# Performance work log

Hardware: AMD Instinct MI355X
Metric: run time of the kernel (lower is better)

The kernel has to match this reference:

```python
import jax, jax.numpy as jnp
import numpy as np

N, E, B = 16384, 131072, 256
F_IN, HID, HEADS, F_CELL, N_OUT = 78, 128, 10, 954, 2
NEG_SLOPE = 0.2  # PyG GATConv default


def setup_inputs() -> dict:
    key = jax.random.key(0)
    ks = jax.random.split(key, 24)
    rn = lambda k, shape, s=0.05: (jax.random.normal(k, shape, jnp.float32) * s)
    inp = {
        "x": rn(ks[0], (N, F_IN), 1.0),
        "edge_index": jax.random.randint(ks[1], (2, E), 0, N, dtype=jnp.int32),
        "batch": (jnp.arange(N, dtype=jnp.int32) // (N // B)),  # 64 nodes per graph, sorted
        "cell": rn(ks[2], (B, F_CELL), 1.0),
        "W1": rn(ks[3], (F_IN, HEADS * HID)),
        "a_src1": rn(ks[4], (HEADS, HID)),
        "a_dst1": rn(ks[5], (HEADS, HID)),
        "b1": jnp.zeros((HEADS * HID,), jnp.float32),
        # GATConv layer 2: 1280 -> 128, 1 head
        "W2": rn(ks[6], (HEADS * HID, HID)),
        "a_src2": rn(ks[7], (1, HID)),
        "a_dst2": rn(ks[8], (1, HID)),
        "b2": jnp.zeros((HID,), jnp.float32),
        # drug1_fc_g1: 128 -> 128
        "Wg": rn(ks[9], (HID, HID)), "bg": jnp.zeros((HID,), jnp.float32),
        # fc head applied to normalized cell (source applies fc1 to cell: 954 -> 2048)
        "Wf1": rn(ks[10], (F_CELL, 2048)), "bf1": jnp.zeros((2048,), jnp.float32),
        "Wf2": rn(ks[11], (2048, 512)), "bf2": jnp.zeros((512,), jnp.float32),
        "Wf3": rn(ks[12], (512, 128)), "bf3": jnp.zeros((128,), jnp.float32),
        "Wo": rn(ks[13], (128, N_OUT)), "bo": jnp.zeros((N_OUT,), jnp.float32),
    }
    return inp


def _gat_layer(xin, src, dst, W, a_s, a_d, b, heads, ch):
    """PyG GATConv: linear -> per-edge leaky_relu(a_src.h_j + a_dst.h_i) ->
    segment softmax over incoming edges of dst -> scatter-add of alpha * h_src."""
    n = xin.shape[0]
    h = (xin @ W).reshape(n, heads, ch)                       # [N,H,C]
    es = jnp.einsum('nhc,hc->nh', h, a_s)                     # alpha_src per node
    ed = jnp.einsum('nhc,hc->nh', h, a_d)                     # alpha_dst per node
    e = jax.nn.leaky_relu(es[src] + ed[dst], NEG_SLOPE)       # [Etot,H]
    m = jax.ops.segment_max(e, dst, num_segments=n)           # stable softmax max
    w = jnp.exp(e - m[dst])                                   # unnormalized alpha
    denom = jax.ops.segment_sum(w, dst, num_segments=n)       # [N,H]
    num = jax.ops.segment_sum(w[:, :, None] * h[src], dst, num_segments=n)  # [N,H,C]
    out = num / denom[:, :, None]
    return out.reshape(n, heads * ch) + b


def reference(x, edge_index, batch, cell, W1, a_src1, a_dst1, b1,
              W2, a_src2, a_dst2, b2, Wg, bg, Wf1, bf1, Wf2, bf2,
              Wf3, bf3, Wo, bo):
    n = x.shape[0]
    # add self-loops (PyG GATConv default)
    loop = jnp.arange(n, dtype=edge_index.dtype)
    src = jnp.concatenate([edge_index[0], loop])
    dst = jnp.concatenate([edge_index[1], loop])

    x1 = jax.nn.elu(_gat_layer(x, src, dst, W1, a_src1, a_dst1, b1, HEADS, HID))
    x1 = jax.nn.elu(_gat_layer(x1, src, dst, W2, a_src2, a_dst2, b2, 1, HID))
    # global max pool over graphs (batch is sorted, all B segments non-empty)
    x1 = jax.ops.segment_max(x1, batch, num_segments=B)       # [B,128]
    x1 = jax.nn.relu(x1 @ Wg + bg)

    # cell branch: L2 normalize rows, then dense head (dropout = identity in eval)
    celln = cell / jnp.maximum(jnp.linalg.norm(cell, axis=1, keepdims=True), 1e-12)
    xc = jax.nn.relu(celln @ Wf1 + bf1)
    xc = jax.nn.relu(xc @ Wf2 + bf2)
    xc = jax.nn.relu(xc @ Wf3 + bf3)
    out = xc @ Wo + bo                                        # [B,2]
    # source returns only `out`; we also expose the (otherwise-dead) GAT branch
    return jnp.concatenate([x1, out], axis=1)                 # [B,130]
```

## Files before the change

kernel.cpp:

```cpp
#include <hip/hip_runtime.h>
#include <hip/hip_bf16.h>
#include <math.h>

#define N_NODES 16384
#define E_EDGES 131072
#define ETOT (E_EDGES + N_NODES)
#define BGRAPH 256
#define F_INPUT 78
#define KPAD1 96
#define HID 128
#define HEADS 10
#define F1 (HEADS * HID)
#define F_CELL 954
#define KPADC 960
#define NEG_SLOPE 0.2f

typedef __attribute__((ext_vector_type(8))) short frag_t;
typedef __attribute__((ext_vector_type(4))) float f4_t;

static __device__ __forceinline__ unsigned fkey(float f) {
    unsigned b = __float_as_uint(f);
    return (b & 0x80000000u) ? ~b : (b | 0x80000000u);
}
static __device__ __forceinline__ float funkey(unsigned k) {
    unsigned b = (k & 0x80000000u) ? (k ^ 0x80000000u) : ~k;
    return __uint_as_float(b);
}
static __device__ __forceinline__ unsigned short f2bf(float f) {
    __hip_bfloat16 h = __float2bfloat16(f);
    return *(unsigned short*)&h;
}
static __device__ __forceinline__ float bf2f(unsigned short u) {
    return __uint_as_float(((unsigned)u) << 16);
}

template<int WM16, int WN16, int OUT_MODE, int ACT, int HAS_BIAS>
__global__ __launch_bounds__(256) void mfma_gemm(
    const unsigned short* __restrict__ A, const unsigned short* __restrict__ BT,
    const float* __restrict__ bias, void* __restrict__ C,
    float* __restrict__ esp, float* __restrict__ edp,
    int M, int N, int Kpad, int lda, int ldc,
    int za, int zb, int zc, int zbias)
{
    constexpr int BM = 32 * WM16, BN = 32 * WN16;
    __shared__ __align__(16) unsigned short Als[BM * 32];
    __shared__ __align__(16) unsigned short Bls[BN * 32];
    const int z = blockIdx.z;
    A  += (size_t)z * za;
    BT += (size_t)z * zb;
    const int t = threadIdx.x;
    const int wave = t >> 6, lane = t & 63;
    const int wr = (wave >> 1) * (16 * WM16);
    const int wc = (wave & 1) * (16 * WN16);
    const int row0 = blockIdx.y * BM;
    const int col0 = blockIdx.x * BN;

    f4_t acc[WM16][WN16];
#pragma unroll
    for (int m = 0; m < WM16; m++)
#pragma unroll
        for (int n = 0; n < WN16; n++) { acc[m][n] = (f4_t){0.f, 0.f, 0.f, 0.f}; }

    const int lrow = lane & 15, kg = lane >> 4;
    for (int kk = 0; kk < Kpad; kk += 32) {
        for (int i = t; i < BM * 4; i += 256) {
            int r = i >> 2, slot = i & 3;
            uint4 v = *(const uint4*)&A[(size_t)(row0 + r) * lda + kk + slot * 8];
            *(uint4*)&Als[r * 32 + ((slot ^ (r & 3) ^ ((r >> 2) & 3)) * 8)] = v;
        }
        for (int i = t; i < BN * 4; i += 256) {
            int r = i >> 2, slot = i & 3;
            uint4 v = *(const uint4*)&BT[(size_t)(col0 + r) * Kpad + kk + slot * 8];
            *(uint4*)&Bls[r * 32 + ((slot ^ (r & 3) ^ ((r >> 2) & 3)) * 8)] = v;
        }
        __syncthreads();
        frag_t af[WM16], bfr[WN16];
#pragma unroll
        for (int m = 0; m < WM16; m++) {
            int r = wr + m * 16 + lrow;
            af[m] = *(frag_t*)&Als[r * 32 + ((kg ^ (r & 3) ^ ((r >> 2) & 3)) * 8)];
        }
#pragma unroll
        for (int n = 0; n < WN16; n++) {
            int r = wc + n * 16 + lrow;
            bfr[n] = *(frag_t*)&Bls[r * 32 + ((kg ^ (r & 3) ^ ((r >> 2) & 3)) * 8)];
        }
#pragma unroll
        for (int m = 0; m < WM16; m++)
#pragma unroll
            for (int n = 0; n < WN16; n++)
                acc[m][n] = __builtin_amdgcn_mfma_f32_16x16x32_bf16(af[m], bfr[n], acc[m][n], 0, 0, 0);
        __syncthreads();
    }

#pragma unroll
    for (int m = 0; m < WM16; m++) {
#pragma unroll
        for (int n = 0; n < WN16; n++) {
            int col = col0 + wc + n * 16 + lrow;
            float bv = HAS_BIAS ? bias[z * zbias + col] : 0.f;
#pragma unroll
            for (int r = 0; r < 4; r++) {
                int row = row0 + wr + m * 16 + kg * 4 + r;
                float v = acc[m][n][r] + bv;
                if (ACT == 1) v = fmaxf(v, 0.f);
                if (ACT == 2) v = (v > 0.f) ? v : expm1f(v);
                size_t ci = (size_t)row * ldc + (size_t)z * zc + col;
                if (OUT_MODE == 0)      ((float*)C)[ci] = v;
                else if (OUT_MODE == 1) ((unsigned short*)C)[ci] = f2bf(v);
                else {
                    if (col < 10)                  esp[row * 10 + col] = v;
                    else if (col >= 16 && col < 26) edp[row * 10 + (col - 16)] = v;
                }
            }
        }
    }
}

#define S0 1572864
#define S1 122880
#define S2 163840
#define S3 1966080
#define S4 1048576
#define S5 65536
#define S6 16384
#define PREP_TOTAL (S0+S1+S2+S3+S4+S5+S6)

__global__ void prep_weights(const float* __restrict__ x,  const float* __restrict__ W1,
                             const float* __restrict__ W2, const float* __restrict__ Wf1,
                             const float* __restrict__ Wf2, const float* __restrict__ Wf3,
                             const float* __restrict__ Wg,
                             unsigned short* __restrict__ xb,  unsigned short* __restrict__ W1T,
                             unsigned short* __restrict__ W2T, unsigned short* __restrict__ Wf1T,
                             unsigned short* __restrict__ Wf2T, unsigned short* __restrict__ Wf3T,
                             unsigned short* __restrict__ WgT)
{
    int i = blockIdx.x * 256 + threadIdx.x;
    if (i < S0) { int r = i / 96, k = i % 96;
        xb[i] = (k < F_INPUT) ? f2bf(x[r * F_INPUT + k]) : 0; return; }
    i -= S0;
    if (i < S1) { int n = i / 96, k = i % 96;
        W1T[i] = (k < F_INPUT) ? f2bf(W1[(size_t)k * F1 + n]) : 0; return; }
    i -= S1;
    if (i < S2) { int n = i / 1280, k = i % 1280;
        W2T[i] = f2bf(W2[(size_t)k * HID + n]); return; }
    i -= S2;
    if (i < S3) { int n = i / 960, k = i % 960;
        Wf1T[i] = (k < F_CELL) ? f2bf(Wf1[(size_t)k * 2048 + n]) : 0; return; }
    i -= S3;
    if (i < S4) { int n = i / 2048, k = i % 2048;
        Wf2T[i] = f2bf(Wf2[(size_t)k * 512 + n]); return; }
    i -= S4;
    if (i < S5) { int n = i / 512, k = i % 512;
        Wf3T[i] = f2bf(Wf3[(size_t)k * HID + n]); return; }
    i -= S5;
    { int n = i / 128, k = i % 128;
        WgT[i] = f2bf(Wg[(size_t)k * HID + n]); }
}

__global__ void fold1_w(const float* __restrict__ W1, const float* __restrict__ as_,
                        const float* __restrict__ ad_, unsigned short* __restrict__ F1T)
{
    int idx = blockIdx.x * 4 + (threadIdx.x >> 6);
    int l = threadIdx.x & 63;
    int r = idx / 96, k = idx % 96;
    int sd = r >> 4, h = r & 15;
    float p = 0.f;
    if (h < HEADS && k < F_INPUT) {
        const float* a = (sd ? ad_ : as_) + h * HID;
        float2 wv = *(const float2*)&W1[(size_t)k * F1 + h * HID + 2 * l];
        float2 av = *(const float2*)&a[2 * l];
        p = wv.x * av.x + wv.y * av.y;
#pragma unroll
        for (int o = 32; o > 0; o >>= 1) p += __shfl_xor(p, o);
    }
    if (l == 0) F1T[(size_t)r * 96 + k] = f2bf(p);
}

__global__ void hist_dst(const int* __restrict__ ei, int* __restrict__ counts)
{
    int e = blockIdx.x * blockDim.x + threadIdx.x;
    if (e >= ETOT) return;
    int dst = (e < E_EDGES) ? ei[E_EDGES + e] : (e - E_EDGES);
    atomicAdd(&counts[dst], 1);
}

__global__ void scan_counts(const int* __restrict__ counts,
                            int* __restrict__ row_start, int* __restrict__ cursor)
{
    __shared__ int part[256];
    int t = threadIdx.x;
    int base = t * 64;
    int sum = 0;
    for (int i = 0; i < 64; i++) sum += counts[base + i];
    part[t] = sum;
    __syncthreads();
    for (int o = 1; o < 256; o <<= 1) {
        int v = 0;
        if (t >= o) v = part[t - o];
        __syncthreads();
        part[t] += v;
        __syncthreads();
    }
    int run = (t == 0) ? 0 : part[t - 1];
    for (int i = 0; i < 64; i++) {
        row_start[base + i] = run;
        cursor[base + i] = run;
        run += counts[base + i];
    }
    if (t == 255) row_start[N_NODES] = run;
}

__global__ void scatter_csr(const int* __restrict__ ei, int* __restrict__ cursor,
                            int* __restrict__ csr_src)
{
    int e = blockIdx.x * blockDim.x + threadIdx.x;
    if (e >= ETOT) return;
    int src, dst;
    if (e < E_EDGES) { src = ei[e]; dst = ei[E_EDGES + e]; } else { src = dst = e - E_EDGES; }
    int pos = atomicAdd(&cursor[dst], 1);
    csr_src[pos] = src;
}

__global__ void attn_coef2(const unsigned short* __restrict__ H2,
                           const float* __restrict__ as_, const float* __restrict__ ad_,
                           float* __restrict__ es, float* __restrict__ ed)
{
    int n = blockIdx.x * 4 + (threadIdx.x >> 6);
    int l = threadIdx.x & 63;
    unsigned p = *(const unsigned*)&H2[(size_t)n * HID + 2 * l];
    float h0 = bf2f((unsigned short)(p & 0xffffu));
    float h1 = bf2f((unsigned short)(p >> 16));
    float2 av = *(const float2*)&as_[2 * l];
    float2 dv = *(const float2*)&ad_[2 * l];
    float vs = h0 * av.x + h1 * av.y;
    float vd = h0 * dv.x + h1 * dv.y;
#pragma unroll
    for (int o = 32; o > 0; o >>= 1) { vs += __shfl_xor(vs, o); vd += __shfl_xor(vd, o); }
    if (l == 0) { es[n] = vs; ed[n] = vd; }
}

__global__ __launch_bounds__(256) void gat1_agg(
    const int* __restrict__ row_start, const int* __restrict__ csr_src,
    const unsigned* __restrict__ xb32,
    const float* __restrict__ es, const float* __restrict__ ed,
    unsigned* __restrict__ aggb)
{
    const int w = threadIdx.x >> 6, l = threadIdx.x & 63;
    const int n = blockIdx.x * 4 + w;
    const int rs = row_start[n];
    const int deg = row_start[n + 1] - rs;

    __shared__ __align__(16) float w_lds[4][64][12];
    __shared__ int src_lds[4][64];

    float edv[HEADS];
    const float* edp = ed + n * HEADS;
#pragma unroll
    for (int h = 0; h < HEADS; h++) edv[h] = edp[h];

    float acc0[HEADS], acc1[HEADS], den[HEADS];
#pragma unroll
    for (int h = 0; h < HEADS; h++) { acc0[h] = 0.f; acc1[h] = 0.f; den[h] = 0.f; }

    for (int base = 0; base < deg; base += 64) {
        int e = base + l;
        int cnt = min(64, deg - base);
        float wv[HEADS];
        if (e < deg) {
            int s = csr_src[rs + e];
            src_lds[w][l] = s;
            const float* ep = es + s * HEADS;
#pragma unroll
            for (int h = 0; h < HEADS; h++) {
                float v = ep[h] + edv[h];
                v = (v >= 0.f) ? v : NEG_SLOPE * v;
                wv[h] = __expf(v);
            }
        } else {
#pragma unroll
            for (int h = 0; h < HEADS; h++) wv[h] = 0.f;
        }
#pragma unroll
        for (int h = 0; h < HEADS; h++) {
            den[h] += wv[h];
            w_lds[w][l][h] = wv[h];
        }
        asm volatile("" ::: "memory");

        for (int j = 0; j < cnt; j++) {
            int sj = src_lds[w][j];
            unsigned xv = 0;
            if (l < 48) xv = xb32[(size_t)sj * 48 + l];
            float x0 = bf2f((unsigned short)(xv & 0xffffu));
            float x1v = bf2f((unsigned short)(xv >> 16));
            float4 wa = *(const float4*)&w_lds[w][j][0];
            float4 wb = *(const float4*)&w_lds[w][j][4];
            float2 wcv = *(const float2*)&w_lds[w][j][8];
            float ww[HEADS] = {wa.x, wa.y, wa.z, wa.w, wb.x, wb.y, wb.z, wb.w, wcv.x, wcv.y};
#pragma unroll
            for (int h = 0; h < HEADS; h++) {
                acc0[h] = fmaf(ww[h], x0, acc0[h]);
                acc1[h] = fmaf(ww[h], x1v, acc1[h]);
            }
        }
        asm volatile("" ::: "memory");
    }

#pragma unroll
    for (int h = 0; h < HEADS; h++)
#pragma unroll
        for (int o = 32; o > 0; o >>= 1) den[h] += __shfl_xor(den[h], o);

    if (l < 48) {
        unsigned* orow = aggb + (size_t)n * 480;
#pragma unroll
        for (int h = 0; h < HEADS; h++) {
            float inv = 1.f / den[h];
            unsigned lo = f2bf(acc0[h] * inv);
            unsigned hi = f2bf(acc1[h] * inv);
            orow[h * 48 + l] = lo | (hi << 16);
        }
    }
}

__global__ __launch_bounds__(256) void gat2_agg(
    const int* __restrict__ row_start, const int* __restrict__ csr_src,
    const unsigned short* __restrict__ H2,
    const float* __restrict__ es, const float* __restrict__ ed,
    const float* __restrict__ b, float* __restrict__ xout)
{
    const int w = threadIdx.x >> 6, l = threadIdx.x & 63;
    const int n = blockIdx.x * 4 + w;
    const int rs = row_start[n];
    const int deg = row_start[n + 1] - rs;
    const float edv = ed[n];

    float2 acc = {0.f, 0.f};
    float den = 0.f;
    for (int base = 0; base < deg; base += 64) {
        int e = base + l;
        int cnt = min(64, deg - base);
        int s = 0;
        float wv = 0.f;
        if (e < deg) {
            s = csr_src[rs + e];
            float v = es[s] + edv;
            v = (v >= 0.f) ? v : NEG_SLOPE * v;
            wv = __expf(v);
        }
        den += wv;
        for (int j = 0; j < cnt; j++) {
            float wj = __shfl(wv, j);
            int   sj = __shfl(s, j);
            unsigned hp = *(const unsigned*)&H2[(size_t)sj * HID + 2 * l];
            acc.x = fmaf(wj, bf2f((unsigned short)(hp & 0xffffu)), acc.x);
            acc.y = fmaf(wj, bf2f((unsigned short)(hp >> 16)), acc.y);
        }
    }
#pragma unroll
    for (int o = 32; o > 0; o >>= 1) den += __shfl_xor(den, o);

    float inv = 1.f / den;
    float2 bv = *(const float2*)&b[2 * l];
    float v0 = acc.x * inv + bv.x;
    float v1 = acc.y * inv + bv.y;
    float2 ov;
    ov.x = (v0 > 0.f) ? v0 : expm1f(v0);
    ov.y = (v1 > 0.f) ? v1 : expm1f(v1);
    *(float2*)(xout + (size_t)n * HID + 2 * l) = ov;
}

__global__ void pool_max(const float* __restrict__ x2, const int* __restrict__ batch,
                         unsigned* __restrict__ pk)
{
    int idx = blockIdx.x * blockDim.x + threadIdx.x;
    if (idx >= N_NODES * HID) return;
    int n = idx >> 7, c = idx & 127;
    atomicMax(&pk[batch[n] * HID + c], fkey(x2[idx]));
}

__global__ void decode_keys_bf16(const unsigned* __restrict__ pk,
                                 unsigned short* __restrict__ outb, int count)
{
    int i = blockIdx.x * blockDim.x + threadIdx.x;
    if (i < count) outb[i] = f2bf(funkey(pk[i]));
}

__global__ void cell_norm(const float* __restrict__ cell, unsigned short* __restrict__ celln)
{
    int b = blockIdx.x;
    int t = threadIdx.x;
    __shared__ float red[256];
    float s = 0.f;
    for (int c = t; c < F_CELL; c += 256) { float v = cell[(size_t)b * F_CELL + c]; s += v * v; }
    red[t] = s; __syncthreads();
    for (int o = 128; o > 0; o >>= 1) { if (t < o) red[t] += red[t + o]; __syncthreads(); }
    float inv = 1.f / fmaxf(sqrtf(red[0]), 1e-12f);
    for (int c = t; c < KPADC; c += 256) {
        float v = (c < F_CELL) ? cell[(size_t)b * F_CELL + c] * inv : 0.f;
        celln[(size_t)b * KPADC + c] = f2bf(v);
    }
}

__global__ void final_out(const float* __restrict__ xg, const float* __restrict__ xc3,
                          const float* __restrict__ Wo, const float* __restrict__ bo,
                          float* __restrict__ out)
{
    int b = blockIdx.x, t = threadIdx.x;
    float v = xc3[b * HID + t];
    float p0 = v * Wo[t * 2], p1 = v * Wo[t * 2 + 1];
    __shared__ float s[4];
#pragma unroll
    for (int o = 32; o > 0; o >>= 1) { p0 += __shfl_down(p0, o); p1 += __shfl_down(p1, o); }
    if ((t & 63) == 0) { s[(t >> 6) * 2] = p0; s[(t >> 6) * 2 + 1] = p1; }
    __syncthreads();
    out[b * 130 + t] = xg[b * HID + t];
    if (t == 0) {
        out[b * 130 + 128] = s[0] + s[2] + bo[0];
        out[b * 130 + 129] = s[1] + s[3] + bo[1];
    }
}

extern "C" void kernel_launch(void* const* d_in, const int* in_sizes, int n_in,
                              void* d_out, int out_size, void* d_ws, size_t ws_size,
                              hipStream_t stream)
{
    const float* x    = (const float*)d_in[0];
    const int*   ei   = (const int*)d_in[1];
    const int*   batch= (const int*)d_in[2];
    const float* cell = (const float*)d_in[3];
    const float* W1   = (const float*)d_in[4];
    const float* as1  = (const float*)d_in[5];
    const float* ad1  = (const float*)d_in[6];
    const float* b1   = (const float*)d_in[7];
    const float* W2   = (const float*)d_in[8];
    const float* as2  = (const float*)d_in[9];
    const float* ad2  = (const float*)d_in[10];
    const float* b2   = (const float*)d_in[11];
    const float* Wg   = (const float*)d_in[12];
    const float* bg   = (const float*)d_in[13];
    const float* Wf1  = (const float*)d_in[14];
    const float* bf1  = (const float*)d_in[15];
    const float* Wf2  = (const float*)d_in[16];
    const float* bf2  = (const float*)d_in[17];
    const float* Wf3  = (const float*)d_in[18];
    const float* bf3  = (const float*)d_in[19];
    const float* Wo   = (const float*)d_in[20];
    const float* bo   = (const float*)d_in[21];
    float* out = (float*)d_out;

    char* w = (char*)d_ws;
    auto alloc = [&](size_t bytes) { char* p = w; w += (bytes + 255) & ~(size_t)255; return p; };
    unsigned short* xb   = (unsigned short*)alloc((size_t)N_NODES * KPAD1 * 2);
    unsigned short* W1T  = (unsigned short*)alloc((size_t)F1 * KPAD1 * 2);
    unsigned short* F1T  = (unsigned short*)alloc((size_t)32 * KPAD1 * 2);
    unsigned*       aggb = (unsigned*)alloc((size_t)N_NODES * 480 * 4);
    unsigned short* x1   = (unsigned short*)alloc((size_t)N_NODES * F1 * 2);
    unsigned short* W2T  = (unsigned short*)alloc((size_t)HID * F1 * 2);
    unsigned short* H2   = (unsigned short*)alloc((size_t)N_NODES * HID * 2);
    float*    es1  = (float*)alloc((size_t)N_NODES * HEADS * 4);
    float*    ed1  = (float*)alloc((size_t)N_NODES * HEADS * 4);
    float*    es2  = (float*)alloc((size_t)N_NODES * 4);
    float*    ed2  = (float*)alloc((size_t)N_NODES * 4);
    float*    x2   = (float*)alloc((size_t)N_NODES * HID * 4);
    int*      counts    = (int*)alloc((size_t)N_NODES * 4);
    int*      row_start = (int*)alloc((size_t)(N_NODES + 1) * 4);
    int*      cursor    = (int*)alloc((size_t)N_NODES * 4);
    int*      csr_src   = (int*)alloc((size_t)ETOT * 4);
    unsigned* pk   = (unsigned*)alloc((size_t)BGRAPH * HID * 4);
    unsigned short* pooledb = (unsigned short*)alloc((size_t)BGRAPH * HID * 2);
    unsigned short* WgT  = (unsigned short*)alloc((size_t)HID * HID * 2);
    float*    xg   = (float*)alloc((size_t)BGRAPH * HID * 4);
    unsigned short* celln = (unsigned short*)alloc((size_t)BGRAPH * KPADC * 2);
    unsigned short* Wf1T = (unsigned short*)alloc((size_t)2048 * KPADC * 2);
    unsigned short* Wf2T = (unsigned short*)alloc((size_t)512 * 2048 * 2);
    unsigned short* Wf3T = (unsigned short*)alloc((size_t)HID * 512 * 2);
    unsigned short* xc1b = (unsigned short*)alloc((size_t)BGRAPH * 2048 * 2);
    unsigned short* xc2b = (unsigned short*)alloc((size_t)BGRAPH * 512 * 2);
    float*    xc3  = (float*)alloc((size_t)BGRAPH * HID * 4);

    hipMemsetAsync(counts, 0, (size_t)N_NODES * 4, stream);
    hipMemsetAsync(pk,     0, (size_t)BGRAPH * HID * 4, stream);

    dim3 b256(256);
    const int egrid = (ETOT + 255) / 256;

    prep_weights<<<PREP_TOTAL / 256, b256, 0, stream>>>(x, W1, W2, Wf1, Wf2, Wf3, Wg,
                                                        xb, W1T, W2T, Wf1T, Wf2T, Wf3T, WgT);
    fold1_w<<<32 * 96 / 4, b256, 0, stream>>>(W1, as1, ad1, F1T);

    hist_dst<<<egrid, b256, 0, stream>>>(ei, counts);
    scan_counts<<<1, b256, 0, stream>>>(counts, row_start, cursor);
    scatter_csr<<<egrid, b256, 0, stream>>>(ei, cursor, csr_src);

    mfma_gemm<4, 1, 2, 0, 0><<<dim3(1, N_NODES / 128), b256, 0, stream>>>(
        xb, F1T, nullptr, nullptr, es1, ed1, N_NODES, 32, KPAD1, KPAD1, 32, 0, 0, 0, 0);
    gat1_agg<<<N_NODES / 4, b256, 0, stream>>>(row_start, csr_src, (const unsigned*)xb,
                                               es1, ed1, aggb);
    mfma_gemm<4, 4, 1, 2, 1><<<dim3(1, N_NODES / 128, HEADS), b256, 0, stream>>>(
        (const unsigned short*)aggb, W1T, b1, x1, nullptr, nullptr,
        N_NODES, HID, KPAD1, 960, F1, KPAD1, HID * KPAD1, HID, HID);

    mfma_gemm<1, 4, 1, 0, 0><<<dim3(1, N_NODES / 32), b256, 0, stream>>>(
        x1, W2T, nullptr, H2, nullptr, nullptr, N_NODES, HID, F1, F1, HID, 0, 0, 0, 0);
    attn_coef2<<<N_NODES / 4, b256, 0, stream>>>(H2, as2, ad2, es2, ed2);
    gat2_agg<<<N_NODES / 4, b256, 0, stream>>>(row_start, csr_src, H2, es2, ed2, b2, x2);

    pool_max<<<(N_NODES * HID + 255) / 256, b256, 0, stream>>>(x2, batch, pk);
    decode_keys_bf16<<<(BGRAPH * HID + 255) / 256, b256, 0, stream>>>(pk, pooledb, BGRAPH * HID);
    mfma_gemm<2, 2, 0, 1, 1><<<dim3(HID / 64, BGRAPH / 64), b256, 0, stream>>>(
        pooledb, WgT, bg, xg, nullptr, nullptr, BGRAPH, HID, HID, HID, HID, 0, 0, 0, 0);

    cell_norm<<<BGRAPH, b256, 0, stream>>>(cell, celln);
    mfma_gemm<2, 2, 1, 1, 1><<<dim3(2048 / 64, BGRAPH / 64), b256, 0, stream>>>(
        celln, Wf1T, bf1, xc1b, nullptr, nullptr, BGRAPH, 2048, KPADC, KPADC, 2048, 0, 0, 0, 0);
    mfma_gemm<1, 2, 1, 1, 1><<<dim3(512 / 64, BGRAPH / 32), b256, 0, stream>>>(
        xc1b, Wf2T, bf2, xc2b, nullptr, nullptr, BGRAPH, 512, 2048, 2048, 512, 0, 0, 0, 0);
    mfma_gemm<2, 2, 0, 1, 1><<<dim3(HID / 64, BGRAPH / 64), b256, 0, stream>>>(
        xc2b, Wf3T, bf3, xc3, nullptr, nullptr, BGRAPH, HID, 512, 512, HID, 0, 0, 0, 0);

    final_out<<<BGRAPH, 128, 0, stream>>>(xg, xc3, Wo, bo, out);
}
```

Before: 250.7 us.

## Fuse epilogues and small kernels to cut launches and intermediate buffers

Merges weight prep, attention-weight folding and buffer zeroing into one launch, which replaces the two memsets. The layer-2 attention coefficients are computed in the W2 GEMM epilogue, and max-pooling moves into the gat2 aggregation through atomicMax. Cell normalization and key decoding share one kernel, and the final 128->2 projection is folded into the Wf3 GEMM epilogue, which writes straight into the output. This removes about six launches and the full x2 round trip through memory, at the cost of shared-memory atomics in the epilogues and more global atomic contention in the pooling.

```diff
diff --git a/kernel.cpp b/kernel.cpp
--- a/kernel.cpp
+++ b/kernel.cpp
@@ -39,6 +39,7 @@
     const unsigned short* __restrict__ A, const unsigned short* __restrict__ BT,
     const float* __restrict__ bias, void* __restrict__ C,
     float* __restrict__ esp, float* __restrict__ edp,
+    const float* __restrict__ ca, const float* __restrict__ cd,
     int M, int N, int Kpad, int lda, int ldc,
     int za, int zb, int zc, int zbias)
 {
@@ -93,26 +94,76 @@
         __syncthreads();
     }
 
-#pragma unroll
-    for (int m = 0; m < WM16; m++) {
-#pragma unroll
-        for (int n = 0; n < WN16; n++) {
-            int col = col0 + wc + n * 16 + lrow;
-            float bv = HAS_BIAS ? bias[z * zbias + col] : 0.f;
-#pragma unroll
-            for (int r = 0; r < 4; r++) {
-                int row = row0 + wr + m * 16 + kg * 4 + r;
-                float v = acc[m][n][r] + bv;
-                if (ACT == 1) v = fmaxf(v, 0.f);
-                if (ACT == 2) v = (v > 0.f) ? v : expm1f(v);
-                size_t ci = (size_t)row * ldc + (size_t)z * zc + col;
-                if (OUT_MODE == 0)      ((float*)C)[ci] = v;
-                else if (OUT_MODE == 1) ((unsigned short*)C)[ci] = f2bf(v);
-                else {
-                    if (col < 10)                  esp[row * 10 + col] = v;
-                    else if (col >= 16 && col < 26) edp[row * 10 + (col - 16)] = v;
+    if constexpr (OUT_MODE <= 2) {
+#pragma unroll
+        for (int m = 0; m < WM16; m++) {
+#pragma unroll
+            for (int n = 0; n < WN16; n++) {
+                int col = col0 + wc + n * 16 + lrow;
+                float bv = HAS_BIAS ? bias[z * zbias + col] : 0.f;
+#pragma unroll
+                for (int r = 0; r < 4; r++) {
+                    int row = row0 + wr + m * 16 + kg * 4 + r;
+                    float v = acc[m][n][r] + bv;
+                    if (ACT == 1) v = fmaxf(v, 0.f);
+                    if (ACT == 2) v = (v > 0.f) ? v : expm1f(v);
+                    size_t ci = (size_t)row * ldc + (size_t)z * zc + col;
+                    if (OUT_MODE == 0)      ((float*)C)[ci] = v;
+                    else if (OUT_MODE == 1) ((unsigned short*)C)[ci] = f2bf(v);
+                    else {
+                        if (col < 10)                  esp[row * 10 + col] = v;
+                        else if (col >= 16 && col < 26) edp[row * 10 + (col - 16)] = v;
+                    }
                 }
             }
+        }
+    } else if constexpr (OUT_MODE == 3) {
+        __shared__ float esl[BM], edl[BM];
+        if (t < BM) { esl[t] = 0.f; edl[t] = 0.f; }
+        __syncthreads();
+#pragma unroll
+        for (int r = 0; r < 4; r++) {
+            int lr = wr + kg * 4 + r;
+            float pes = 0.f, ped = 0.f;
+#pragma unroll
+            for (int n = 0; n < WN16; n++) {
+                int col = col0 + wc + n * 16 + lrow;
+                float v = acc[0][n][r];
+                ((unsigned short*)C)[(size_t)(row0 + lr) * ldc + col] = f2bf(v);
+                pes = fmaf(v, ca[col], pes);
+                ped = fmaf(v, cd[col], ped);
+            }
+            atomicAdd(&esl[lr], pes);
+            atomicAdd(&edl[lr], ped);
+        }
+        __syncthreads();
+        if (t < BM) { esp[row0 + t] = esl[t]; edp[row0 + t] = edl[t]; }
+    } else {
+        __shared__ float o2l[BM][2];
+        if (t < BM) { o2l[t][0] = 0.f; o2l[t][1] = 0.f; }
+        __syncthreads();
+#pragma unroll
+        for (int m = 0; m < WM16; m++) {
+#pragma unroll
+            for (int r = 0; r < 4; r++) {
+                int lr = wr + m * 16 + kg * 4 + r;
+                float p0 = 0.f, p1 = 0.f;
+#pragma unroll
+                for (int n = 0; n < WN16; n++) {
+                    int col = col0 + wc + n * 16 + lrow;
+                    float v = acc[m][n][r] + (HAS_BIAS ? bias[col] : 0.f);
+                    if (ACT == 1) v = fmaxf(v, 0.f);
+                    p0 = fmaf(v, ca[col * 2], p0);
+                    p1 = fmaf(v, ca[col * 2 + 1], p1);
+                }
+                atomicAdd(&o2l[lr][0], p0);
+                atomicAdd(&o2l[lr][1], p1);
+            }
+        }
+        __syncthreads();
+        if (t < BM) {
+            ((float*)C)[(size_t)(row0 + t) * ldc + 128] = o2l[t][0] + cd[0];
+            ((float*)C)[(size_t)(row0 + t) * ldc + 129] = o2l[t][1] + cd[1];
         }
     }
 }
@@ -125,56 +176,69 @@
 #define S5 65536
 #define S6 16384
 #define PREP_TOTAL (S0+S1+S2+S3+S4+S5+S6)
-
-__global__ void prep_weights(const float* __restrict__ x,  const float* __restrict__ W1,
-                             const float* __restrict__ W2, const float* __restrict__ Wf1,
-                             const float* __restrict__ Wf2, const float* __restrict__ Wf3,
-                             const float* __restrict__ Wg,
-                             unsigned short* __restrict__ xb,  unsigned short* __restrict__ W1T,
-                             unsigned short* __restrict__ W2T, unsigned short* __restrict__ Wf1T,
-                             unsigned short* __restrict__ Wf2T, unsigned short* __restrict__ Wf3T,
-                             unsigned short* __restrict__ WgT)
-{
-    int i = blockIdx.x * 256 + threadIdx.x;
-    if (i < S0) { int r = i / 96, k = i % 96;
-        xb[i] = (k < F_INPUT) ? f2bf(x[r * F_INPUT + k]) : 0; return; }
-    i -= S0;
-    if (i < S1) { int n = i / 96, k = i % 96;
-        W1T[i] = (k < F_INPUT) ? f2bf(W1[(size_t)k * F1 + n]) : 0; return; }
-    i -= S1;
-    if (i < S2) { int n = i / 1280, k = i % 1280;
-        W2T[i] = f2bf(W2[(size_t)k * HID + n]); return; }
-    i -= S2;
-    if (i < S3) { int n = i / 960, k = i % 960;
-        Wf1T[i] = (k < F_CELL) ? f2bf(Wf1[(size_t)k * 2048 + n]) : 0; return; }
-    i -= S3;
-    if (i < S4) { int n = i / 2048, k = i % 2048;
-        Wf2T[i] = f2bf(Wf2[(size_t)k * 512 + n]); return; }
-    i -= S4;
-    if (i < S5) { int n = i / 512, k = i % 512;
-        Wf3T[i] = f2bf(Wf3[(size_t)k * HID + n]); return; }
-    i -= S5;
-    { int n = i / 128, k = i % 128;
-        WgT[i] = f2bf(Wg[(size_t)k * HID + n]); }
-}
-
-__global__ void fold1_w(const float* __restrict__ W1, const float* __restrict__ as_,
-                        const float* __restrict__ ad_, unsigned short* __restrict__ F1T)
-{
-    int idx = blockIdx.x * 4 + (threadIdx.x >> 6);
-    int l = threadIdx.x & 63;
-    int r = idx / 96, k = idx % 96;
-    int sd = r >> 4, h = r & 15;
-    float p = 0.f;
-    if (h < HEADS && k < F_INPUT) {
-        const float* a = (sd ? ad_ : as_) + h * HID;
-        float2 wv = *(const float2*)&W1[(size_t)k * F1 + h * HID + 2 * l];
-        float2 av = *(const float2*)&a[2 * l];
-        p = wv.x * av.x + wv.y * av.y;
-#pragma unroll
-        for (int o = 32; o > 0; o >>= 1) p += __shfl_xor(p, o);
-    }
-    if (l == 0) F1T[(size_t)r * 96 + k] = f2bf(p);
+#define NB_ELEM (PREP_TOTAL / 256)
+#define NB_FOLD 768
+#define NB_ZCNT 64
+#define NB_ZPK  128
+
+__global__ void prep_all(const float* __restrict__ x,  const float* __restrict__ W1,
+                         const float* __restrict__ W2, const float* __restrict__ Wf1,
+                         const float* __restrict__ Wf2, const float* __restrict__ Wf3,
+                         const float* __restrict__ Wg,
+                         const float* __restrict__ as1, const float* __restrict__ ad1,
+                         unsigned short* __restrict__ xb,  unsigned short* __restrict__ W1T,
+                         unsigned short* __restrict__ W2T, unsigned short* __restrict__ Wf1T,
+                         unsigned short* __restrict__ Wf2T, unsigned short* __restrict__ Wf3T,
+                         unsigned short* __restrict__ WgT, unsigned short* __restrict__ F1T,
+                         int* __restrict__ counts, unsigned* __restrict__ pk)
+{
+    int blk = blockIdx.x, t = threadIdx.x;
+    if (blk < NB_ELEM) {
+        int i = blk * 256 + t;
+        if (i < S0) { int r = i / 96, k = i % 96;
+            xb[i] = (k < F_INPUT) ? f2bf(x[r * F_INPUT + k]) : 0; return; }
+        i -= S0;
+        if (i < S1) { int n = i / 96, k = i % 96;
+            W1T[i] = (k < F_INPUT) ? f2bf(W1[(size_t)k * F1 + n]) : 0; return; }
+        i -= S1;
+        if (i < S2) { int n = i / 1280, k = i % 1280;
+            W2T[i] = f2bf(W2[(size_t)k * HID + n]); return; }
+        i -= S2;
+        if (i < S3) { int n = i / 960, k = i % 960;
+            Wf1T[i] = (k < F_CELL) ? f2bf(Wf1[(size_t)k * 2048 + n]) : 0; return; }
+        i -= S3;
+        if (i < S4) { int n = i / 2048, k = i % 2048;
+            Wf2T[i] = f2bf(Wf2[(size_t)k * 512 + n]); return; }
+        i -= S4;
+        if (i < S5) { int n = i / 512, k = i % 512;
+            Wf3T[i] = f2bf(Wf3[(size_t)k * HID + n]); return; }
+        i -= S5;
+        { int n = i / 128, k = i % 128;
+            WgT[i] = f2bf(Wg[(size_t)k * HID + n]); }
+        return;
+    }
+    blk -= NB_ELEM;
+    if (blk < NB_FOLD) {
+        int idx = blk * 4 + (t >> 6);
+        int l = t & 63;
+        int r = idx / 96, k = idx % 96;
+        int sd = r >> 4, h = r & 15;
+        float p = 0.f;
+        if (h < HEADS && k < F_INPUT) {
+            const float* a = (sd ? ad1 : as1) + h * HID;
+            float2 wv = *(const float2*)&W1[(size_t)k * F1 + h * HID + 2 * l];
+            float2 av = *(const float2*)&a[2 * l];
+            p = wv.x * av.x + wv.y * av.y;
+#pragma unroll
+            for (int o = 32; o > 0; o >>= 1) p += __shfl_xor(p, o);
+        }
+        if (l == 0) F1T[(size_t)r * 96 + k] = f2bf(p);
+        return;
+    }
+    blk -= NB_FOLD;
+    if (blk < NB_ZCNT) { counts[blk * 256 + t] = 0; return; }
+    blk -= NB_ZCNT;
+    pk[blk * 256 + t] = 0;
 }
 
 __global__ void hist_dst(const int* __restrict__ ei, int* __restrict__ counts)
@@ -222,24 +286,6 @@
     csr_src[pos] = src;
 }
 
-__global__ void attn_coef2(const unsigned short* __restrict__ H2,
-                           const float* __restrict__ as_, const float* __restrict__ ad_,
-                           float* __restrict__ es, float* __restrict__ ed)
-{
-    int n = blockIdx.x * 4 + (threadIdx.x >> 6);
-    int l = threadIdx.x & 63;
-    unsigned p = *(const unsigned*)&H2[(size_t)n * HID + 2 * l];
-    float h0 = bf2f((unsigned short)(p & 0xffffu));
-    float h1 = bf2f((unsigned short)(p >> 16));
-    float2 av = *(const float2*)&as_[2 * l];
-    float2 dv = *(const float2*)&ad_[2 * l];
-    float vs = h0 * av.x + h1 * av.y;
-    float vd = h0 * dv.x + h1 * dv.y;
-#pragma unroll
-    for (int o = 32; o > 0; o >>= 1) { vs += __shfl_xor(vs, o); vd += __shfl_xor(vd, o); }
-    if (l == 0) { es[n] = vs; ed[n] = vd; }
-}
-
 __global__ __launch_bounds__(256) void gat1_agg(
     const int* __restrict__ row_start, const int* __restrict__ csr_src,
     const unsigned* __restrict__ xb32,
@@ -328,7 +374,8 @@
     const int* __restrict__ row_start, const int* __restrict__ csr_src,
     const unsigned short* __restrict__ H2,
     const float* __restrict__ es, const float* __restrict__ ed,
-    const float* __restrict__ b, float* __restrict__ xout)
+    const float* __restrict__ b, const int* __restrict__ batch,
+    unsigned* __restrict__ pk)
 {
     const int w = threadIdx.x >> 6, l = threadIdx.x & 63;
     const int n = blockIdx.x * 4 + w;
@@ -365,60 +412,34 @@
     float2 bv = *(const float2*)&b[2 * l];
     float v0 = acc.x * inv + bv.x;
     float v1 = acc.y * inv + bv.y;
-    float2 ov;
-    ov.x = (v0 > 0.f) ? v0 : expm1f(v0);
-    ov.y = (v1 > 0.f) ? v1 : expm1f(v1);
-    *(float2*)(xout + (size_t)n * HID + 2 * l) = ov;
-}
-
-__global__ void pool_max(const float* __restrict__ x2, const int* __restrict__ batch,
-                         unsigned* __restrict__ pk)
-{
-    int idx = blockIdx.x * blockDim.x + threadIdx.x;
-    if (idx >= N_NODES * HID) return;
-    int n = idx >> 7, c = idx & 127;
-    atomicMax(&pk[batch[n] * HID + c], fkey(x2[idx]));
-}
-
-__global__ void decode_keys_bf16(const unsigned* __restrict__ pk,
-                                 unsigned short* __restrict__ outb, int count)
-{
-    int i = blockIdx.x * blockDim.x + threadIdx.x;
-    if (i < count) outb[i] = f2bf(funkey(pk[i]));
-}
-
-__global__ void cell_norm(const float* __restrict__ cell, unsigned short* __restrict__ celln)
-{
-    int b = blockIdx.x;
+    v0 = (v0 > 0.f) ? v0 : expm1f(v0);
+    v1 = (v1 > 0.f) ? v1 : expm1f(v1);
+    int g = batch[n];
+    atomicMax(&pk[g * HID + 2 * l], fkey(v0));
+    atomicMax(&pk[g * HID + 2 * l + 1], fkey(v1));
+}
+
+__global__ void decode_cell(const unsigned* __restrict__ pk,
+                            unsigned short* __restrict__ pooledb,
+                            const float* __restrict__ cell,
+                            unsigned short* __restrict__ celln)
+{
     int t = threadIdx.x;
-    __shared__ float red[256];
-    float s = 0.f;
-    for (int c = t; c < F_CELL; c += 256) { float v = cell[(size_t)b * F_CELL + c]; s += v * v; }
-    red[t] = s; __syncthreads();
-    for (int o = 128; o > 0; o >>= 1) { if (t < o) red[t] += red[t + o]; __syncthreads(); }
-    float inv = 1.f / fmaxf(sqrtf(red[0]), 1e-12f);
-    for (int c = t; c < KPADC; c += 256) {
-        float v = (c < F_CELL) ? cell[(size_t)b * F_CELL + c] * inv : 0.f;
-        celln[(size_t)b * KPADC + c] = f2bf(v);
-    }
-}
-
-__global__ void final_out(const float* __restrict__ xg, const float* __restrict__ xc3,
-                          const float* __restrict__ Wo, const float* __restrict__ bo,
-                          float* __restrict__ out)
-{
-    int b = blockIdx.x, t = threadIdx.x;
-    float v = xc3[b * HID + t];
-    float p0 = v * Wo[t * 2], p1 = v * Wo[t * 2 + 1];
-    __shared__ float s[4];
-#pragma unroll
-    for (int o = 32; o > 0; o >>= 1) { p0 += __shfl_down(p0, o); p1 += __shfl_down(p1, o); }
-    if ((t & 63) == 0) { s[(t >> 6) * 2] = p0; s[(t >> 6) * 2 + 1] = p1; }
-    __syncthreads();
-    out[b * 130 + t] = xg[b * HID + t];
-    if (t == 0) {
-        out[b * 130 + 128] = s[0] + s[2] + bo[0];
-        out[b * 130 + 129] = s[1] + s[3] + bo[1];
+    if (blockIdx.x < BGRAPH) {
+        int b = blockIdx.x;
+        __shared__ float red[256];
+        float s = 0.f;
+        for (int c = t; c < F_CELL; c += 256) { float v = cell[(size_t)b * F_CELL + c]; s += v * v; }
+        red[t] = s; __syncthreads();
+        for (int o = 128; o > 0; o >>= 1) { if (t < o) red[t] += red[t + o]; __syncthreads(); }
+        float inv = 1.f / fmaxf(sqrtf(red[0]), 1e-12f);
+        for (int c = t; c < KPADC; c += 256) {
+            float v = (c < F_CELL) ? cell[(size_t)b * F_CELL + c] * inv : 0.f;
+            celln[(size_t)b * KPADC + c] = f2bf(v);
+        }
+    } else {
+        int i = (blockIdx.x - BGRAPH) * 256 + t;
+        if (i < BGRAPH * HID) pooledb[i] = f2bf(funkey(pk[i]));
     }
 }
 
@@ -463,7 +484,6 @@
     float*    ed1  = (float*)alloc((size_t)N_NODES * HEADS * 4);
     float*    es2  = (float*)alloc((size_t)N_NODES * 4);
     float*    ed2  = (float*)alloc((size_t)N_NODES * 4);
-    float*    x2   = (float*)alloc((size_t)N_NODES * HID * 4);
     int*      counts    = (int*)alloc((size_t)N_NODES * 4);
     int*      row_start = (int*)alloc((size_t)(N_NODES + 1) * 4);
     int*      cursor    = (int*)alloc((size_t)N_NODES * 4);
@@ -471,54 +491,57 @@
     unsigned* pk   = (unsigned*)alloc((size_t)BGRAPH * HID * 4);
     unsigned short* pooledb = (unsigned short*)alloc((size_t)BGRAPH * HID * 2);
     unsigned short* WgT  = (unsigned short*)alloc((size_t)HID * HID * 2);
-    float*    xg   = (float*)alloc((size_t)BGRAPH * HID * 4);
     unsigned short* celln = (unsigned short*)alloc((size_t)BGRAPH * KPADC * 2);
     unsigned short* Wf1T = (unsigned short*)alloc((size_t)2048 * KPADC * 2);
     unsigned short* Wf2T = (unsigned short*)alloc((size_t)512 * 2048 * 2);
     unsigned short* Wf3T = (unsigned short*)alloc((size_t)HID * 512 * 2);
     unsigned short* xc1b = (unsigned short*)alloc((size_t)BGRAPH * 2048 * 2);
     unsigned short* xc2b = (unsigned short*)alloc((size_t)BGRAPH * 512 * 2);
-    float*    xc3  = (float*)alloc((size_t)BGRAPH * HID * 4);
-
-    hipMemsetAsync(counts, 0, (size_t)N_NODES * 4, stream);
-    hipMemsetAsync(pk,     0, (size_t)BGRAPH * HID * 4, stream);
 
     dim3 b256(256);
     const int egrid = (ETOT + 255) / 256;
 
-    prep_weights<<<PREP_TOTAL / 256, b256, 0, stream>>>(x, W1, W2, Wf1, Wf2, Wf3, Wg,
-                                                        xb, W1T, W2T, Wf1T, Wf2T, Wf3T, WgT);
-    fold1_w<<<32 * 96 / 4, b256, 0, stream>>>(W1, as1, ad1, F1T);
+    prep_all<<<NB_ELEM + NB_FOLD + NB_ZCNT + NB_ZPK, b256, 0, stream>>>(
+        x, W1, W2, Wf1, Wf2, Wf3, Wg, as1, ad1,
+        xb, W1T, W2T, Wf1T, Wf2T, Wf3T, WgT, F1T, counts, pk);
 
     hist_dst<<<egrid, b256, 0, stream>>>(ei, counts);
     scan_counts<<<1, b256, 0, stream>>>(counts, row_start, cursor);
     scatter_csr<<<egrid, b256, 0, stream>>>(ei, cursor, csr_src);
 
     mfma_gemm<4, 1, 2, 0, 0><<<dim3(1, N_NODES / 128), b256, 0, stream>>>(
-        xb, F1T, nullptr, nullptr, es1, ed1, N_NODES, 32, KPAD1, KPAD1, 32, 0, 0, 0, 0);
+        xb, F1T, nullptr, nullptr, es1, ed1, nullptr, nullptr,
+        N_NODES, 32, KPAD1, KPAD1, 32, 0, 0, 0, 0);
+
     gat1_agg<<<N_NODES / 4, b256, 0, stream>>>(row_start, csr_src, (const unsigned*)xb,
                                                es1, ed1, aggb);
+
     mfma_gemm<4, 4, 1, 2, 1><<<dim3(1, N_NODES / 128, HEADS), b256, 0, stream>>>(
-        (const unsigned short*)aggb, W1T, b1, x1, nullptr, nullptr,
+        (const unsigned short*)aggb, W1T, b1, x1, nullptr, nullptr, nullptr, nullptr,
         N_NODES, HID, KPAD1, 960, F1, KPAD1, HID * KPAD1, HID, HID);
 
-    mfma_gemm<1, 4, 1, 0, 0><<<dim3(1, N_NODES / 32), b256, 0, stream>>>(
-        x1, W2T, nullptr, H2, nullptr, nullptr, N_NODES, HID, F1, F1, HID, 0, 0, 0, 0);
-    attn_coef2<<<N_NODES / 4, b256, 0, stream>>>(H2, as2, ad2, es2, ed2);
-    gat2_agg<<<N_NODES / 4, b256, 0, stream>>>(row_start, csr_src, H2, es2, ed2, b2, x2);
-
-    pool_max<<<(N_NODES * HID + 255) / 256, b256, 0, stream>>>(x2, batch, pk);
-    decode_keys_bf16<<<(BGRAPH * HID + 255) / 256, b256, 0, stream>>>(pk, pooledb, BGRAPH * HID);
+    mfma_gemm<1, 4, 3, 0, 0><<<dim3(1, N_NODES / 32), b256, 0, stream>>>(
+        x1, W2T, nullptr, H2, es2, ed2, as2, ad2,
+        N_NODES, HID, F1, F1, HID, 0, 0, 0, 0);
+
+    gat2_agg<<<N_NODES / 4, b256, 0, stream>>>(row_start, csr_src, H2, es2, ed2, b2,
+                                               batch, pk);
+
+    decode_cell<<<BGRAPH + (BGRAPH * HID + 255) / 256, b256, 0, stream>>>(
+        pk, pooledb, cell, celln);
+
     mfma_gemm<2, 2, 0, 1, 1><<<dim3(HID / 64, BGRAPH / 64), b256, 0, stream>>>(
-        pooledb, WgT, bg, xg, nullptr, nullptr, BGRAPH, HID, HID, HID, HID, 0, 0, 0, 0);
-
-    cell_norm<<<BGRAPH, b256, 0, stream>>>(cell, celln);
+        pooledb, WgT, bg, out, nullptr, nullptr, nullptr, nullptr,
+        BGRAPH, HID, HID, HID, 130, 0, 0, 0, 0);
+
     mfma_gemm<2, 2, 1, 1, 1><<<dim3(2048 / 64, BGRAPH / 64), b256, 0, stream>>>(
-        celln, Wf1T, bf1, xc1b, nullptr, nullptr, BGRAPH, 2048, KPADC, KPADC, 2048, 0, 0, 0, 0);
+        celln, Wf1T, bf1, xc1b, nullptr, nullptr, nullptr, nullptr,
+        BGRAPH, 2048, KPADC, KPADC, 2048, 0, 0, 0, 0);
     mfma_gemm<1, 2, 1, 1, 1><<<dim3(512 / 64, BGRAPH / 32), b256, 0, stream>>>(
-        xc1b, Wf2T, bf2, xc2b, nullptr, nullptr, BGRAPH, 512, 2048, 2048, 512, 0, 0, 0, 0);
-    mfma_gemm<2, 2, 0, 1, 1><<<dim3(HID / 64, BGRAPH / 64), b256, 0, stream>>>(
-        xc2b, Wf3T, bf3, xc3, nullptr, nullptr, BGRAPH, HID, 512, 512, HID, 0, 0, 0, 0);
-
-    final_out<<<BGRAPH, 128, 0, stream>>>(xg, xc3, Wo, bo, out);
-}
+        xc1b, Wf2T, bf2, xc2b, nullptr, nullptr, nullptr, nullptr,
+        BGRAPH, 512, 2048, 2048, 512, 0, 0, 0, 0);
+
+    mfma_gemm<2, 4, 4, 1, 1><<<dim3(1, BGRAPH / 64), b256, 0, stream>>>(
+        xc2b, Wf3T, bf3, out, nullptr, nullptr, Wo, bo,
+        BGRAPH, HID, 512, 512, 130, 0, 0, 0, 0);
+}
```

Measured after the change: 253.1 us. About the same (+0.9%).
